# Kernel optimization log

Measured on AMD Instinct MI355X. Metric: run time of the kernel, lower is better.

The kernel has to match this reference:

```python
import jax, jax.numpy as jnp
import numpy as np

N_NODES = 8192
TOP_K = 32


def setup_inputs() -> dict:
    key = jax.random.key(0)
    k1, k2 = jax.random.split(key)
    scores = jax.random.normal(k1, (N_NODES, N_NODES), dtype=jnp.float32)
    # Gumbel(phi, 1).sample() == phi + Gumbel(0, 1) noise; materialize noise here.
    gumbel_noise = jax.random.gumbel(k2, (N_NODES, N_NODES), dtype=jnp.float32)
    tau = jnp.float32(0.5)
    return {"scores": scores, "gumbel_noise": gumbel_noise, "tau": tau, "k": TOP_K}


def reference(scores, gumbel_noise, tau, k):
    phi = scores / tau                      # [N, N]
    gumbels = phi + gumbel_noise            # reparameterized Gumbel(phi, 1) sample
    _, ind = jax.lax.top_k(gumbels, k)      # [N, k] indices along last dim
    rows = jnp.arange(scores.shape[0])[:, None]
    khot = jnp.zeros_like(gumbels).at[rows, ind].set(1.0)  # k-hot mask [N, N]
    soft = jax.nn.softmax(phi, axis=-1)
    # straight-through: forward = khot, gradient flows through softmax
    return khot + soft - jax.lax.stop_gradient(soft)
```

## Files before the change

kernel.cpp:

```cpp
#include <hip/hip_runtime.h>
#include <stdint.h>


namespace {

constexpr int kN = 8192;
constexpr int kThreads = 256;
constexpr int kVPT = kN / (kThreads * 4);
constexpr int kEPT = kN / kThreads;

typedef float f32x4 __attribute__((ext_vector_type(4)));

__device__ __forceinline__ uint32_t f2sortable(float x) {
  uint32_t b = __float_as_uint(x);
  return (b & 0x80000000u) ? ~b : (b | 0x80000000u);
}

__global__ __launch_bounds__(kThreads, 4) void st_topk_khot(
    const float* __restrict__ scores, const float* __restrict__ noise,
    const float* __restrict__ tau_p, const int* __restrict__ k_p,
    float* __restrict__ out) {
  __shared__ uint32_t sdata[kN];
  __shared__ uint32_t hist[kThreads];
  __shared__ uint32_t cum[kThreads + 1];
  __shared__ uint32_t bcast[3];

  const int t = threadIdx.x;
  const size_t row = blockIdx.x;
  const float tau = tau_p[0];
  const uint32_t k = (uint32_t)k_p[0];

  const float4* s4 = reinterpret_cast<const float4*>(scores + row * (size_t)kN);
  const float4* g4 = reinterpret_cast<const float4*>(noise + row * (size_t)kN);
  uint4* sd4 = reinterpret_cast<uint4*>(sdata);

  uint32_t u[kEPT];

#pragma unroll
  for (int i = 0; i < kVPT; ++i) {
    const int vi = i * kThreads + t;
    float4 s = s4[vi];
    float4 g = g4[vi];
    uint4 q;
    q.x = f2sortable(s.x / tau + g.x);
    q.y = f2sortable(s.y / tau + g.y);
    q.z = f2sortable(s.z / tau + g.z);
    q.w = f2sortable(s.w / tau + g.w);
    u[i * 4 + 0] = q.x;
    u[i * 4 + 1] = q.y;
    u[i * 4 + 2] = q.z;
    u[i * 4 + 3] = q.w;
    sd4[vi] = q;
  }

  uint32_t prefix = 0, pmask = 0, desired = k, eq = 0;

#pragma unroll
  for (int pass = 0; pass < 4; ++pass) {
    const int shift = 24 - pass * 8;
    hist[t] = 0;
    __syncthreads();

    if (pass == 0) {
#pragma unroll
      for (int e = 0; e < kEPT; ++e) {
        const uint32_t b = u[e] >> 24;
        uint64_t m = ~0ull;
#pragma unroll
        for (int bit = 0; bit < 8; ++bit) {
          const uint64_t bal = __ballot((int)((b >> bit) & 1u));
          m &= ((b >> bit) & 1u) ? bal : ~bal;
        }
        if ((threadIdx.x & 63) == __builtin_ctzll(m))
          atomicAdd(&hist[b], (uint32_t)__popcll(m));
      }
    } else {
#pragma unroll
      for (int e = 0; e < kEPT; ++e) {
        if ((u[e] & pmask) == prefix)
          atomicAdd(&hist[(u[e] >> shift) & 255u], 1u);
      }
    }
    __syncthreads();

    cum[t] = hist[t];
    if (t == 0) cum[kThreads] = 0;
#pragma unroll
    for (int off = 1; off < kThreads; off <<= 1) {
      __syncthreads();
      const uint32_t add = (t + off < kThreads) ? cum[t + off] : 0u;
      __syncthreads();
      cum[t] += add;
    }
    __syncthreads();

    const uint32_t cb = cum[t];
    const uint32_t cb1 = cum[t + 1];
    if (cb >= desired && cb1 < desired) {
      bcast[0] = prefix | ((uint32_t)t << shift);
      bcast[1] = desired - cb1;
      bcast[2] = cb - cb1;
    }
    __syncthreads();
    prefix = bcast[0];
    desired = bcast[1];
    eq = bcast[2];
    pmask |= 0xFFu << shift;
    __syncthreads();
  }

  const uint32_t thr = prefix;

  if (eq != desired) {
    if (t == 0) {
      uint32_t need = desired;
      for (int j = 0; j < kN; ++j) {
        if (sdata[j] == thr) {
          if (need) {
            --need;
          } else {
            sdata[j] = 0u;
          }
        }
      }
    }
    __syncthreads();
#pragma unroll
    for (int i = 0; i < kVPT; ++i) {
      uint4 q = sd4[i * kThreads + t];
      u[i * 4 + 0] = q.x;
      u[i * 4 + 1] = q.y;
      u[i * 4 + 2] = q.z;
      u[i * 4 + 3] = q.w;
    }
  }

  f32x4* o4 = reinterpret_cast<f32x4*>(out + row * (size_t)kN);
#pragma unroll
  for (int i = 0; i < kVPT; ++i) {
    const int vi = i * kThreads + t;
    f32x4 o;
    o.x = (u[i * 4 + 0] >= thr) ? 1.0f : 0.0f;
    o.y = (u[i * 4 + 1] >= thr) ? 1.0f : 0.0f;
    o.z = (u[i * 4 + 2] >= thr) ? 1.0f : 0.0f;
    o.w = (u[i * 4 + 3] >= thr) ? 1.0f : 0.0f;
    __builtin_nontemporal_store(o, o4 + vi);
  }
}

}

extern "C" void kernel_launch(void* const* d_in, const int* in_sizes, int n_in,
                              void* d_out, int out_size, void* d_ws, size_t ws_size,
                              hipStream_t stream) {
  (void)in_sizes;
  (void)n_in;
  (void)d_ws;
  (void)ws_size;
  (void)out_size;
  const float* scores = (const float*)d_in[0];
  const float* noise = (const float*)d_in[1];
  const float* tau_p = (const float*)d_in[2];
  const int* k_p = (const int*)d_in[3];
  float* out = (float*)d_out;

  hipLaunchKernelGGL(st_topk_khot, dim3(kN), dim3(kThreads), 0, stream,
                     scores, noise, tau_p, k_p, out);
}
```

Measured before the change: 630.4 us.

## Use 10-bit first radix pass with candidate compaction and drop row staging in LDS

Replaces the 4x8-bit radix select with a 1024-bin first pass, then compacts the candidates matching that prefix into a small shared list, so the later passes scan only those candidates. The 32 KB per-row shared buffer is gone and launch bounds rise to 8 blocks per CU to raise occupancy. Prefix sums now use wave shuffles instead of a sync-heavy shared-memory scan. The serial tie-breaking by a single thread is replaced by a parallel prefix-count over equal keys. This adds more atomic contention on the first histogram and needs a fallback path when the candidate list overflows.

```diff
diff --git a/kernel.cpp b/kernel.cpp
--- a/kernel.cpp
+++ b/kernel.cpp
@@ -8,6 +8,8 @@
 constexpr int kThreads = 256;
 constexpr int kVPT = kN / (kThreads * 4);
 constexpr int kEPT = kN / kThreads;
+constexpr int kBins0 = 1024;
+constexpr uint32_t kCap = 1024;
 
 typedef float f32x4 __attribute__((ext_vector_type(4)));
 
@@ -16,23 +18,25 @@
   return (b & 0x80000000u) ? ~b : (b | 0x80000000u);
 }
 
-__global__ __launch_bounds__(kThreads, 4) void st_topk_khot(
+__global__ __launch_bounds__(kThreads, 8) void st_topk_khot(
     const float* __restrict__ scores, const float* __restrict__ noise,
     const float* __restrict__ tau_p, const int* __restrict__ k_p,
     float* __restrict__ out) {
-  __shared__ uint32_t sdata[kN];
-  __shared__ uint32_t hist[kThreads];
-  __shared__ uint32_t cum[kThreads + 1];
+  __shared__ __align__(16) uint32_t hist[kBins0];
+  __shared__ uint32_t clist[kCap];
+  __shared__ uint32_t wsum[4];
   __shared__ uint32_t bcast[3];
+  __shared__ uint32_t cnt;
 
   const int t = threadIdx.x;
+  const int lane = t & 63;
+  const int w = t >> 6;
   const size_t row = blockIdx.x;
   const float tau = tau_p[0];
   const uint32_t k = (uint32_t)k_p[0];
 
   const float4* s4 = reinterpret_cast<const float4*>(scores + row * (size_t)kN);
   const float4* g4 = reinterpret_cast<const float4*>(noise + row * (size_t)kN);
-  uint4* sd4 = reinterpret_cast<uint4*>(sdata);
 
   uint32_t u[kEPT];
 
@@ -41,110 +45,170 @@
     const int vi = i * kThreads + t;
     float4 s = s4[vi];
     float4 g = g4[vi];
-    uint4 q;
-    q.x = f2sortable(s.x / tau + g.x);
-    q.y = f2sortable(s.y / tau + g.y);
-    q.z = f2sortable(s.z / tau + g.z);
-    q.w = f2sortable(s.w / tau + g.w);
-    u[i * 4 + 0] = q.x;
-    u[i * 4 + 1] = q.y;
-    u[i * 4 + 2] = q.z;
-    u[i * 4 + 3] = q.w;
-    sd4[vi] = q;
-  }
-
-  uint32_t prefix = 0, pmask = 0, desired = k, eq = 0;
-
-#pragma unroll
-  for (int pass = 0; pass < 4; ++pass) {
-    const int shift = 24 - pass * 8;
-    hist[t] = 0;
-    __syncthreads();
-
-    if (pass == 0) {
-#pragma unroll
-      for (int e = 0; e < kEPT; ++e) {
-        const uint32_t b = u[e] >> 24;
-        uint64_t m = ~0ull;
-#pragma unroll
-        for (int bit = 0; bit < 8; ++bit) {
-          const uint64_t bal = __ballot((int)((b >> bit) & 1u));
-          m &= ((b >> bit) & 1u) ? bal : ~bal;
-        }
-        if ((threadIdx.x & 63) == __builtin_ctzll(m))
-          atomicAdd(&hist[b], (uint32_t)__popcll(m));
+    u[i * 4 + 0] = f2sortable(s.x / tau + g.x);
+    u[i * 4 + 1] = f2sortable(s.y / tau + g.y);
+    u[i * 4 + 2] = f2sortable(s.z / tau + g.z);
+    u[i * 4 + 3] = f2sortable(s.w / tau + g.w);
+  }
+
+  reinterpret_cast<uint4*>(hist)[t] = uint4{0u, 0u, 0u, 0u};
+  if (t == 0) cnt = 0u;
+  __syncthreads();
+#pragma unroll
+  for (int e = 0; e < kEPT; ++e) atomicAdd(&hist[u[e] >> 22], 1u);
+  __syncthreads();
+
+  uint32_t prefix, desired, eqn;
+
+  {
+    uint4 hv = reinterpret_cast<const uint4*>(hist)[t];
+    const uint32_t l0 = hv.x, l1 = hv.y, l2 = hv.z, l3 = hv.w;
+    const uint32_t lsum = l0 + l1 + l2 + l3;
+    uint32_t inc = lsum;
+#pragma unroll
+    for (int off = 1; off < 64; off <<= 1) {
+      const uint32_t o = __shfl_down(inc, off);
+      if (lane + off < 64) inc += o;
+    }
+    if (lane == 0) wsum[w] = inc;
+    __syncthreads();
+    uint32_t hi = 0;
+#pragma unroll
+    for (int ww = 0; ww < 4; ++ww)
+      if (ww > w) hi += wsum[ww];
+    const uint32_t S = hi + (inc - lsum);
+    const uint32_t c3 = S + l3, c2 = c3 + l2, c1 = c2 + l1, c0 = c1 + l0;
+    const uint32_t cums[4] = {c0, c1, c2, c3};
+    const uint32_t nxts[4] = {c1, c2, c3, S};
+    const uint32_t lv[4] = {l0, l1, l2, l3};
+#pragma unroll
+    for (int e = 0; e < 4; ++e) {
+      if (cums[e] >= k && nxts[e] < k) {
+        bcast[0] = (uint32_t)(4 * t + e) << 22;
+        bcast[1] = k - nxts[e];
+        bcast[2] = lv[e];
+      }
+    }
+  }
+  __syncthreads();
+  prefix = bcast[0];
+  desired = bcast[1];
+  eqn = bcast[2];
+
+#pragma unroll
+  for (int e = 0; e < kEPT; ++e) {
+    if ((u[e] & 0xFFC00000u) == prefix) {
+      const uint32_t pos = atomicAdd(&cnt, 1u);
+      if (pos < kCap) clist[pos] = u[e];
+    }
+  }
+  __syncthreads();
+  const uint32_t m = cnt;
+  const bool ovf = (m > kCap);
+  uint32_t pmask = 0xFFC00000u;
+
+  const int shifts[3] = {14, 6, 0};
+  const uint32_t dmasks[3] = {255u, 255u, 63u};
+#pragma unroll
+  for (int p = 0; p < 3; ++p) {
+    const int shift = shifts[p];
+    const uint32_t dmask = dmasks[p];
+    hist[t] = 0u;
+    __syncthreads();
+    if (!ovf) {
+      for (uint32_t idx = t; idx < m; idx += kThreads) {
+        const uint32_t key = clist[idx];
+        if ((key & pmask) == prefix) atomicAdd(&hist[(key >> shift) & dmask], 1u);
       }
     } else {
 #pragma unroll
-      for (int e = 0; e < kEPT; ++e) {
-        if ((u[e] & pmask) == prefix)
-          atomicAdd(&hist[(u[e] >> shift) & 255u], 1u);
-      }
-    }
-    __syncthreads();
-
-    cum[t] = hist[t];
-    if (t == 0) cum[kThreads] = 0;
-#pragma unroll
-    for (int off = 1; off < kThreads; off <<= 1) {
-      __syncthreads();
-      const uint32_t add = (t + off < kThreads) ? cum[t + off] : 0u;
-      __syncthreads();
-      cum[t] += add;
-    }
-    __syncthreads();
-
-    const uint32_t cb = cum[t];
-    const uint32_t cb1 = cum[t + 1];
-    if (cb >= desired && cb1 < desired) {
+      for (int e = 0; e < kEPT; ++e)
+        if ((u[e] & pmask) == prefix) atomicAdd(&hist[(u[e] >> shift) & dmask], 1u);
+    }
+    __syncthreads();
+    const uint32_t lsum = hist[t];
+    uint32_t inc = lsum;
+#pragma unroll
+    for (int off = 1; off < 64; off <<= 1) {
+      const uint32_t o = __shfl_down(inc, off);
+      if (lane + off < 64) inc += o;
+    }
+    if (lane == 0) wsum[w] = inc;
+    __syncthreads();
+    uint32_t hi = 0;
+#pragma unroll
+    for (int ww = 0; ww < 4; ++ww)
+      if (ww > w) hi += wsum[ww];
+    const uint32_t S = hi + (inc - lsum);
+    const uint32_t cum = S + lsum;
+    if (cum >= desired && S < desired) {
       bcast[0] = prefix | ((uint32_t)t << shift);
-      bcast[1] = desired - cb1;
-      bcast[2] = cb - cb1;
+      bcast[1] = desired - S;
+      bcast[2] = lsum;
     }
     __syncthreads();
     prefix = bcast[0];
     desired = bcast[1];
-    eq = bcast[2];
-    pmask |= 0xFFu << shift;
+    eqn = bcast[2];
+    pmask |= dmask << shift;
     __syncthreads();
   }
 
   const uint32_t thr = prefix;
-
-  if (eq != desired) {
-    if (t == 0) {
-      uint32_t need = desired;
-      for (int j = 0; j < kN; ++j) {
-        if (sdata[j] == thr) {
-          if (need) {
-            --need;
-          } else {
-            sdata[j] = 0u;
-          }
-        }
-      }
-    }
-    __syncthreads();
+  f32x4* o4 = reinterpret_cast<f32x4*>(out + row * (size_t)kN);
+
+  if (eqn == desired) {
 #pragma unroll
     for (int i = 0; i < kVPT; ++i) {
-      uint4 q = sd4[i * kThreads + t];
-      u[i * 4 + 0] = q.x;
-      u[i * 4 + 1] = q.y;
-      u[i * 4 + 2] = q.z;
-      u[i * 4 + 3] = q.w;
-    }
-  }
-
-  f32x4* o4 = reinterpret_cast<f32x4*>(out + row * (size_t)kN);
-#pragma unroll
-  for (int i = 0; i < kVPT; ++i) {
-    const int vi = i * kThreads + t;
-    f32x4 o;
-    o.x = (u[i * 4 + 0] >= thr) ? 1.0f : 0.0f;
-    o.y = (u[i * 4 + 1] >= thr) ? 1.0f : 0.0f;
-    o.z = (u[i * 4 + 2] >= thr) ? 1.0f : 0.0f;
-    o.w = (u[i * 4 + 3] >= thr) ? 1.0f : 0.0f;
-    __builtin_nontemporal_store(o, o4 + vi);
+      f32x4 o;
+      o.x = (u[i * 4 + 0] >= thr) ? 1.0f : 0.0f;
+      o.y = (u[i * 4 + 1] >= thr) ? 1.0f : 0.0f;
+      o.z = (u[i * 4 + 2] >= thr) ? 1.0f : 0.0f;
+      o.w = (u[i * 4 + 3] >= thr) ? 1.0f : 0.0f;
+      __builtin_nontemporal_store(o, o4 + (i * kThreads + t));
+    }
+  } else {
+    uint32_t keep = 0u;
+    uint32_t base = 0u;
+#pragma unroll
+    for (int i = 0; i < kVPT; ++i) {
+      const uint32_t f0 = (u[i * 4 + 0] == thr) ? 1u : 0u;
+      const uint32_t f1 = (u[i * 4 + 1] == thr) ? 1u : 0u;
+      const uint32_t f2 = (u[i * 4 + 2] == thr) ? 1u : 0u;
+      const uint32_t f3 = (u[i * 4 + 3] == thr) ? 1u : 0u;
+      const uint32_t lc = f0 + f1 + f2 + f3;
+      uint32_t pf = lc;
+#pragma unroll
+      for (int off = 1; off < 64; off <<= 1) {
+        const uint32_t o = __shfl_up(pf, off);
+        if (lane >= off) pf += o;
+      }
+      if (lane == 63) wsum[w] = pf;
+      __syncthreads();
+      uint32_t lower = 0, total = 0;
+#pragma unroll
+      for (int ww = 0; ww < 4; ++ww) {
+        const uint32_t v = wsum[ww];
+        total += v;
+        if (ww < w) lower += v;
+      }
+      uint32_t r = base + lower + (pf - lc);
+      if (f0) { if (r < desired) keep |= 1u << (i * 4 + 0); ++r; }
+      if (f1) { if (r < desired) keep |= 1u << (i * 4 + 1); ++r; }
+      if (f2) { if (r < desired) keep |= 1u << (i * 4 + 2); ++r; }
+      if (f3) { if (r < desired) keep |= 1u << (i * 4 + 3); ++r; }
+      base += total;
+      __syncthreads();
+    }
+#pragma unroll
+    for (int i = 0; i < kVPT; ++i) {
+      f32x4 o;
+      o.x = (u[i * 4 + 0] > thr || (u[i * 4 + 0] == thr && ((keep >> (i * 4 + 0)) & 1u))) ? 1.0f : 0.0f;
+      o.y = (u[i * 4 + 1] > thr || (u[i * 4 + 1] == thr && ((keep >> (i * 4 + 1)) & 1u))) ? 1.0f : 0.0f;
+      o.z = (u[i * 4 + 2] > thr || (u[i * 4 + 2] == thr && ((keep >> (i * 4 + 2)) & 1u))) ? 1.0f : 0.0f;
+      o.w = (u[i * 4 + 3] > thr || (u[i * 4 + 3] == thr && ((keep >> (i * 4 + 3)) & 1u))) ? 1.0f : 0.0f;
+      __builtin_nontemporal_store(o, o4 + (i * kThreads + t));
+    }
   }
 }
 
```

New measurement: 674.1 us. +6.9%, slower.
